# Performance work log

Measured on AMD Instinct MI355X. Metric: run time of the kernel, lower is better.

Reference implementation:

```python
import jax, jax.numpy as jnp
import numpy as np

HEAD_SIZE = 64
N_EMBD = 1024
B, T = 8, 2048

def setup_inputs() -> dict:
    key = jax.random.key(0)
    kx, kq, kk, kv = jax.random.split(key, 4)
    x = jax.random.normal(kx, (B, T, N_EMBD), dtype=jnp.float32)
    s = 1.0 / np.sqrt(N_EMBD)
    Wq = jax.random.normal(kq, (N_EMBD, HEAD_SIZE), dtype=jnp.float32) * s
    Wk = jax.random.normal(kk, (N_EMBD, HEAD_SIZE), dtype=jnp.float32) * s
    Wv = jax.random.normal(kv, (N_EMBD, HEAD_SIZE), dtype=jnp.float32) * s
    return {"x": x, "Wq": Wq, "Wk": Wk, "Wv": Wv}

def reference(x, Wq, Wk, Wv):
    # x: [B,T,C]; project to q,k,v: [B,T,H]
    q = jnp.einsum('btc,ch->bth', x, Wq)
    k = jnp.einsum('btc,ch->bth', x, Wk)
    v = jnp.einsum('btc,ch->bth', x, Wv)
    scale = 1.0 / jnp.sqrt(jnp.asarray(HEAD_SIZE, dtype=x.dtype))
    wei = jnp.einsum('bth,bsh->bts', q, k) * scale  # [B,T,T]
    Tlen = x.shape[1]
    causal = jnp.tril(jnp.ones((Tlen, Tlen), dtype=bool))
    wei = jnp.where(causal[None, :, :], wei, jnp.asarray(-jnp.inf, dtype=wei.dtype))
    wei = jax.nn.softmax(wei, axis=-1)
    # dropout p=0.0 (eval) -> identity
    out = jnp.einsum('bts,bsh->bth', wei, v)  # [B,T,H]
    return out
```

## Files before the change

kernel.cpp:

```cpp
#include <hip/hip_runtime.h>
#include <math.h>

static constexpr int BN = 8;
static constexpr int TS = 2048;
static constexpr int CE = 1024;
static constexpr int HD = 64;

typedef __attribute__((ext_vector_type(8))) short bf16x8;
typedef __attribute__((ext_vector_type(4))) float f32x4;

typedef __attribute__((address_space(3))) void lds_void;
typedef __attribute__((address_space(1))) void glb_void;

__device__ __forceinline__ unsigned short f2bf(float f) {
    union { float f; unsigned u; } v; v.f = f;
    unsigned r = v.u + 0x7FFF + ((v.u >> 16) & 1);
    return (unsigned short)(r >> 16);
}

__device__ __forceinline__ bf16x8 pack8(const float4& a, const float4& b) {
    union { unsigned u[4]; bf16x8 v; } r;
    asm("v_cvt_pk_bf16_f32 %0, %1, %2" : "=v"(r.u[0]) : "v"(a.x), "v"(a.y));
    asm("v_cvt_pk_bf16_f32 %0, %1, %2" : "=v"(r.u[1]) : "v"(a.z), "v"(a.w));
    asm("v_cvt_pk_bf16_f32 %0, %1, %2" : "=v"(r.u[2]) : "v"(b.x), "v"(b.y));
    asm("v_cvt_pk_bf16_f32 %0, %1, %2" : "=v"(r.u[3]) : "v"(b.z), "v"(b.w));
    return r.v;
}

__global__ __launch_bounds__(256) void wt_kernel(
    const float* __restrict__ Wq, const float* __restrict__ Wk,
    const float* __restrict__ Wv, unsigned short* __restrict__ Wt)
{
    __shared__ float T[64 * 69];
    const int tid = threadIdx.x;
    const int m  = blockIdx.x >> 4;
    const int kt = blockIdx.x & 15;
    const float* W = (m == 0) ? Wq : (m == 1) ? Wk : Wv;
    const int k0 = kt * 64;

    #pragma unroll
    for (int it = 0; it < 4; ++it) {
        int idx = tid + it * 256;
        int r = idx >> 4, nq = idx & 15;
        float4 v = *(const float4*)(W + (long)(k0 + r) * HD + nq * 4);
        T[r * 69 + nq * 4 + 0] = v.x;
        T[r * 69 + nq * 4 + 1] = v.y;
        T[r * 69 + nq * 4 + 2] = v.z;
        T[r * 69 + nq * 4 + 3] = v.w;
    }
    __syncthreads();
    #pragma unroll
    for (int it = 0; it < 2; ++it) {
        int idx = tid + it * 256;
        int n = idx >> 3, kq = idx & 7;
        unsigned short h[8];
        #pragma unroll
        for (int s = 0; s < 8; ++s)
            h[s] = f2bf(T[(kq * 8 + s) * 69 + n]);
        *(uint4*)(Wt + (long)(m * 64 + n) * CE + k0 + kq * 8) = *(uint4*)h;
    }
}

static constexpr int NTI = CE / 64;

__global__ __launch_bounds__(512, 1) void qkv_mfma_kernel(
    const float* __restrict__ x, const unsigned short* __restrict__ Wt,
    unsigned short* __restrict__ qo, unsigned short* __restrict__ ko,
    unsigned short* __restrict__ vo)
{
    __shared__ __align__(16) float          xR[4][32 * 64];
    __shared__ __align__(16) unsigned short wR[4][192 * 64];

    const int tid = threadIdx.x;
    const int l  = tid & 63;
    const int v  = tid >> 6;
    const int lr = l & 15, h = l >> 4;
    const int wr = v >> 2;
    const int wc = v & 3;
    const long row0 = (long)blockIdx.x * 32;

    const int sr = tid >> 4;
    const int gd = tid & 15;
    const float* xsrc = x + (row0 + sr) * CE + (gd ^ (2 * (sr & 7))) * 4;
    const int xdst = v << 8;

    const unsigned short* wsrc0; const unsigned short* wsrc1;
    const unsigned short* wsrc2;
    int wdst0, wdst1, wdst2;
    {
        int G, rw, g8;
        G = tid;        rw = G >> 3; g8 = G & 7;
        wsrc0 = Wt + (long)rw * CE + (g8 ^ (rw & 7)) * 8;
        wdst0 = (0 * 512 + v * 64) * 8;
        G = 512 + tid;  rw = G >> 3; g8 = G & 7;
        wsrc1 = Wt + (long)rw * CE + (g8 ^ (rw & 7)) * 8;
        wdst1 = (1 * 512 + v * 64) * 8;
        G = 1024 + tid; rw = G >> 3; g8 = G & 7;
        wsrc2 = Wt + (long)rw * CE + (g8 ^ (rw & 7)) * 8;
        wdst2 = (2 * 512 + v * 64) * 8;
    }

    f32x4 acc[3];
    #pragma unroll
    for (int j = 0; j < 3; ++j) acc[j] = (f32x4){0.f, 0.f, 0.f, 0.f};

    #define STAGE(nb, t) do {                                                 \
        __builtin_amdgcn_global_load_lds((const glb_void*)(xsrc + (t) * 64),  \
            (lds_void*)(&xR[nb][xdst]), 16, 0, 0);                            \
        __builtin_amdgcn_global_load_lds((const glb_void*)(wsrc0 + (t) * 64), \
            (lds_void*)(&wR[nb][wdst0]), 16, 0, 0);                           \
        __builtin_amdgcn_global_load_lds((const glb_void*)(wsrc1 + (t) * 64), \
            (lds_void*)(&wR[nb][wdst1]), 16, 0, 0);                           \
        __builtin_amdgcn_global_load_lds((const glb_void*)(wsrc2 + (t) * 64), \
            (lds_void*)(&wR[nb][wdst2]), 16, 0, 0);                           \
        __builtin_amdgcn_sched_barrier(0); } while (0)

    #define COMPUTE(cb) do {                                                  \
        _Pragma("unroll")                                                     \
        for (int kk = 0; kk < 2; ++kk) {                                      \
            const int xg = (kk * 8 + 2 * h) ^ (2 * (lr & 7));                 \
            const float* ap = &xR[cb][(16 * wr + lr) * 64 + xg * 4];          \
            float4 a0 = *(const float4*)ap;                                   \
            float4 a1 = *(const float4*)(ap + 4);                             \
            bf16x8 af = pack8(a0, a1);                                        \
            _Pragma("unroll")                                                 \
            for (int j = 0; j < 3; ++j) {                                     \
                const int rwj = 48 * wc + 16 * j + lr;                        \
                const int wg  = (kk * 4 + h) ^ (lr & 7);                      \
                bf16x8 bf = *(const bf16x8*)(&wR[cb][rwj * 64 + wg * 8]);     \
                acc[j] = __builtin_amdgcn_mfma_f32_16x16x32_bf16(             \
                    af, bf, acc[j], 0, 0, 0);                                 \
            }                                                                 \
        } } while (0)

    STAGE(0, 0);
    STAGE(1, 1);
    STAGE(2, 2);

    #pragma unroll
    for (int t = 0; t < NTI; ++t) {
        const int cb = t & 3;
        if (t + 3 < NTI) STAGE((t + 3) & 3, t + 3);
        if      (t <  NTI - 3) asm volatile("s_waitcnt vmcnt(12)" ::: "memory");
        else if (t == NTI - 3) asm volatile("s_waitcnt vmcnt(8)"  ::: "memory");
        else if (t == NTI - 2) asm volatile("s_waitcnt vmcnt(4)"  ::: "memory");
        else                   asm volatile("s_waitcnt vmcnt(0)"  ::: "memory");
        __builtin_amdgcn_s_barrier();
        asm volatile("" ::: "memory");
        COMPUTE(cb);
        __builtin_amdgcn_s_barrier();
    }
    #undef STAGE
    #undef COMPUTE

    #pragma unroll
    for (int j = 0; j < 3; ++j) {
        const int n0 = 48 * wc + 16 * j;
        if (n0 < 128) {
            unsigned short* outp = (n0 < 64) ? qo : ko;
            const int h0 = (n0 & 63) + lr;
            #pragma unroll
            for (int r = 0; r < 4; ++r) {
                long rowg = row0 + 16 * wr + h * 4 + r;
                outp[rowg * HD + h0] = f2bf(acc[j][r]);
            }
        } else {
            const int d  = (n0 - 128) + lr;
            const int bb = (int)(row0 >> 11);
            const int t0 = (int)(row0 & 2047) + 16 * wr + h * 4;
            unsigned short h4[4];
            #pragma unroll
            for (int r = 0; r < 4; ++r) h4[r] = f2bf(acc[j][r]);
            *(uint2*)(vo + (((long)(bb * 64 + d)) << 11) + t0) = *(uint2*)h4;
        }
    }
}

__global__ __launch_bounds__(256) void attn_mfma_kernel(
    const unsigned short* __restrict__ qg,
    const unsigned short* __restrict__ kg,
    const unsigned short* __restrict__ vtg,
    float* __restrict__ out)
{
    __shared__ unsigned short Pl[4][32 * 72];
    __shared__ float Ow[4][32 * 64];
    __shared__ float Ml[4][32], Ll[4][32];

    const int tid = threadIdx.x;
    const int w  = tid >> 6;
    const int l  = tid & 63;
    const int lr = l & 15, h = l >> 4;
    const int b  = blockIdx.x >> 5;
    const int pr = blockIdx.x & 31;

    const unsigned short* qB = qg  + (long)b * TS * HD;
    const unsigned short* kB = kg  + (long)b * TS * HD;
    const unsigned short* vT = vtg + (long)b * HD * TS;
    float* outB = out + (long)b * TS * HD;

    unsigned short* Pw = &Pl[w][0];

    for (int half = 0; half < 2; ++half) {
        const int qt = half ? (63 - pr) : pr;
        const int q0 = qt * 32;
        const int NT = (qt + 2) >> 1;

        bf16x8 Qf[2][2];
        #pragma unroll
        for (int qf = 0; qf < 2; ++qf)
            #pragma unroll
            for (int ks = 0; ks < 2; ++ks)
                Qf[qf][ks] = *(const bf16x8*)(qB + (q0 + 16 * qf + lr) * HD + 32 * ks + 8 * h);

        f32x4 O[2][4];
        #pragma unroll
        for (int rf = 0; rf < 2; ++rf)
            #pragma unroll
            for (int cf = 0; cf < 4; ++cf)
                O[rf][cf] = (f32x4){0.f, 0.f, 0.f, 0.f};
        float mrow[2] = {-1e30f, -1e30f};
        float lrow[2] = {0.f, 0.f};

        for (int kt = w; kt < NT; kt += 4) {
            const int key0 = kt * 64;
            bf16x8 Kf[4][2], Vf[4][2];
            #pragma unroll
            for (int kf = 0; kf < 4; ++kf)
                #pragma unroll
                for (int ks = 0; ks < 2; ++ks)
                    Kf[kf][ks] = *(const bf16x8*)(kB + (key0 + 16 * kf + lr) * HD + 32 * ks + 8 * h);
            #pragma unroll
            for (int cf = 0; cf < 4; ++cf)
                #pragma unroll
                for (int ks = 0; ks < 2; ++ks)
                    Vf[cf][ks] = *(const bf16x8*)(vT + (16 * cf + lr) * TS + key0 + 32 * ks + 8 * h);

            f32x4 st[4][2];
            #pragma unroll
            for (int kf = 0; kf < 4; ++kf)
                #pragma unroll
                for (int qf = 0; qf < 2; ++qf)
                    st[kf][qf] = (f32x4){0.f, 0.f, 0.f, 0.f};
            #pragma unroll
            for (int ks = 0; ks < 2; ++ks)
                #pragma unroll
                for (int kf = 0; kf < 4; ++kf)
                    #pragma unroll
                    for (int qf = 0; qf < 2; ++qf)
                        st[kf][qf] = __builtin_amdgcn_mfma_f32_16x16x32_bf16(
                            Kf[kf][ks], Qf[qf][ks], st[kf][qf], 0, 0, 0);

            const bool lastt = (kt == NT - 1);
            float alpha[2];
            #pragma unroll
            for (int qf = 0; qf < 2; ++qf) {
                const int qrow = q0 + 16 * qf + lr;
                float tm = -1e30f;
                #pragma unroll
                for (int kf = 0; kf < 4; ++kf)
                    #pragma unroll
                    for (int r = 0; r < 4; ++r) {
                        float sv = st[kf][qf][r] * 0.125f;
                        if (lastt && (key0 + 16 * kf + 4 * h + r) > qrow) sv = -1e30f;
                        st[kf][qf][r] = sv;
                        tm = fmaxf(tm, sv);
                    }
                tm = fmaxf(tm, __shfl_xor(tm, 16));
                tm = fmaxf(tm, __shfl_xor(tm, 32));
                const float mn = fmaxf(mrow[qf], tm);
                alpha[qf] = __expf(mrow[qf] - mn);
                mrow[qf] = mn;
                float rs = 0.f;
                #pragma unroll
                for (int kf = 0; kf < 4; ++kf)
                    #pragma unroll
                    for (int r = 0; r < 4; ++r) {
                        float p = __expf(st[kf][qf][r] - mn);
                        st[kf][qf][r] = p;
                        rs += p;
                    }
                rs += __shfl_xor(rs, 16);
                rs += __shfl_xor(rs, 32);
                lrow[qf] = lrow[qf] * alpha[qf] + rs;
                #pragma unroll
                for (int kf = 0; kf < 4; ++kf) {
                    unsigned a01 = (unsigned)f2bf(st[kf][qf][0]) |
                                   ((unsigned)f2bf(st[kf][qf][1]) << 16);
                    unsigned a23 = (unsigned)f2bf(st[kf][qf][2]) |
                                   ((unsigned)f2bf(st[kf][qf][3]) << 16);
                    unsigned short* pp = Pw + (16 * qf + lr) * 72 + 16 * kf + 4 * h;
                    *(unsigned*)(pp)     = a01;
                    *(unsigned*)(pp + 2) = a23;
                }
            }

            #pragma unroll
            for (int rf = 0; rf < 2; ++rf)
                #pragma unroll
                for (int r = 0; r < 4; ++r) {
                    float aO = __shfl(alpha[rf], 4 * h + r);
                    #pragma unroll
                    for (int cf = 0; cf < 4; ++cf)
                        O[rf][cf][r] *= aO;
                }

            bf16x8 pa[2][2];
            #pragma unroll
            for (int rf = 0; rf < 2; ++rf)
                #pragma unroll
                for (int ks = 0; ks < 2; ++ks)
                    pa[rf][ks] = *(const bf16x8*)(Pw + (16 * rf + lr) * 72 + 32 * ks + 8 * h);
            #pragma unroll
            for (int ks = 0; ks < 2; ++ks)
                #pragma unroll
                for (int rf = 0; rf < 2; ++rf)
                    #pragma unroll
                    for (int cf = 0; cf < 4; ++cf)
                        O[rf][cf] = __builtin_amdgcn_mfma_f32_16x16x32_bf16(
                            pa[rf][ks], Vf[cf][ks], O[rf][cf], 0, 0, 0);
        }

        #pragma unroll
        for (int rf = 0; rf < 2; ++rf)
            #pragma unroll
            for (int cf = 0; cf < 4; ++cf)
                #pragma unroll
                for (int r = 0; r < 4; ++r)
                    Ow[w][(16 * rf + 4 * h + r) * 64 + 16 * cf + lr] = O[rf][cf][r];
        if (h == 0) {
            #pragma unroll
            for (int qf = 0; qf < 2; ++qf) {
                Ml[w][16 * qf + lr] = mrow[qf];
                Ll[w][16 * qf + lr] = lrow[qf];
            }
        }
        __syncthreads();

        {
            const int q  = tid >> 3;
            const int d0 = (tid & 7) * 8;
            float mM = -1e30f;
            #pragma unroll
            for (int w2 = 0; w2 < 4; ++w2) mM = fmaxf(mM, Ml[w2][q]);
            float lS = 0.f;
            float a8[8] = {0.f,0.f,0.f,0.f,0.f,0.f,0.f,0.f};
            #pragma unroll
            for (int w2 = 0; w2 < 4; ++w2) {
                float sc = __expf(Ml[w2][q] - mM);
                lS += Ll[w2][q] * sc;
                #pragma unroll
                for (int e = 0; e < 8; ++e)
                    a8[e] += sc * Ow[w2][q * 64 + d0 + e];
            }
            const float inv = 1.f / lS;
            float4 o1 = {a8[0]*inv, a8[1]*inv, a8[2]*inv, a8[3]*inv};
            float4 o2 = {a8[4]*inv, a8[5]*inv, a8[6]*inv, a8[7]*inv};
            *(float4*)(outB + (long)(q0 + q) * HD + d0)     = o1;
            *(float4*)(outB + (long)(q0 + q) * HD + d0 + 4) = o2;
        }
        __syncthreads();
    }
}

extern "C" void kernel_launch(void* const* d_in, const int* in_sizes, int n_in,
                              void* d_out, int out_size, void* d_ws, size_t ws_size,
                              hipStream_t stream) {
    const float* x  = (const float*)d_in[0];
    const float* Wq = (const float*)d_in[1];
    const float* Wk = (const float*)d_in[2];
    const float* Wv = (const float*)d_in[3];
    float* out = (float*)d_out;

    const size_t nqkv = (size_t)BN * TS * HD;
    unsigned short* qb = (unsigned short*)d_ws;
    unsigned short* kb = qb + nqkv;
    unsigned short* vt = kb + nqkv;

    unsigned short* Wt = (unsigned short*)d_out;

    wt_kernel<<<48, 256, 0, stream>>>(Wq, Wk, Wv, Wt);
    qkv_mfma_kernel<<<(BN * TS) / 32, 512, 0, stream>>>(x, Wt, qb, kb, vt);
    attn_mfma_kernel<<<BN * 32, 256, 0, stream>>>(qb, kb, vt, out);
}
```

Before: 61.01 us.

## Double QKV projection row tile to 64 and switch to triple-buffered LDS pipeline

The QKV projection kernel now handles 64 rows of x per block instead of 32, so each wave computes two 16-row MFMA tiles that share every loaded weight fragment. This halves how often the bf16 weight tile is re-fetched from global memory and halves the block count to 256. The LDS ring drops from 4 to 3 buffers, the x swizzle changes, and the next stage is issued after the second barrier instead of before compute. In exchange there are fewer blocks to spread across CUs and a shorter prefetch lead.

```diff
diff --git a/kernel.cpp b/kernel.cpp
--- a/kernel.cpp
+++ b/kernel.cpp
@@ -68,8 +68,8 @@
     unsigned short* __restrict__ qo, unsigned short* __restrict__ ko,
     unsigned short* __restrict__ vo)
 {
-    __shared__ __align__(16) float          xR[4][32 * 64];
-    __shared__ __align__(16) unsigned short wR[4][192 * 64];
+    __shared__ __align__(16) float          xR[3][64 * 64];
+    __shared__ __align__(16) unsigned short wR[3][192 * 64];
 
     const int tid = threadIdx.x;
     const int l  = tid & 63;
@@ -77,59 +77,75 @@
     const int lr = l & 15, h = l >> 4;
     const int wr = v >> 2;
     const int wc = v & 3;
-    const long row0 = (long)blockIdx.x * 32;
-
-    const int sr = tid >> 4;
-    const int gd = tid & 15;
-    const float* xsrc = x + (row0 + sr) * CE + (gd ^ (2 * (sr & 7))) * 4;
-    const int xdst = v << 8;
+    const long row0 = (long)blockIdx.x * 64;
+
+    const float* xsrc0; const float* xsrc1;
+    {
+        int G, r_, gd;
+        G = tid;        r_ = G >> 4; gd = G & 15;
+        xsrc0 = x + (row0 + r_) * CE + (gd ^ (r_ & 15)) * 4;
+        G = 512 + tid;  r_ = G >> 4; gd = G & 15;
+        xsrc1 = x + (row0 + r_) * CE + (gd ^ (r_ & 15)) * 4;
+    }
+    const int xd0 = 256 * v;
+    const int xd1 = 2048 + 256 * v;
 
     const unsigned short* wsrc0; const unsigned short* wsrc1;
     const unsigned short* wsrc2;
-    int wdst0, wdst1, wdst2;
     {
         int G, rw, g8;
-        G = tid;        rw = G >> 3; g8 = G & 7;
+        G = tid;         rw = G >> 3; g8 = G & 7;
         wsrc0 = Wt + (long)rw * CE + (g8 ^ (rw & 7)) * 8;
-        wdst0 = (0 * 512 + v * 64) * 8;
-        G = 512 + tid;  rw = G >> 3; g8 = G & 7;
+        G = 512 + tid;   rw = G >> 3; g8 = G & 7;
         wsrc1 = Wt + (long)rw * CE + (g8 ^ (rw & 7)) * 8;
-        wdst1 = (1 * 512 + v * 64) * 8;
-        G = 1024 + tid; rw = G >> 3; g8 = G & 7;
+        G = 1024 + tid;  rw = G >> 3; g8 = G & 7;
         wsrc2 = Wt + (long)rw * CE + (g8 ^ (rw & 7)) * 8;
-        wdst2 = (2 * 512 + v * 64) * 8;
-    }
-
-    f32x4 acc[3];
+    }
+    const int wd0 = 512 * v;
+    const int wd1 = 4096 + 512 * v;
+    const int wd2 = 8192 + 512 * v;
+
+    f32x4 acc[2][3];
     #pragma unroll
-    for (int j = 0; j < 3; ++j) acc[j] = (f32x4){0.f, 0.f, 0.f, 0.f};
+    for (int i = 0; i < 2; ++i)
+        #pragma unroll
+        for (int j = 0; j < 3; ++j)
+            acc[i][j] = (f32x4){0.f, 0.f, 0.f, 0.f};
 
     #define STAGE(nb, t) do {                                                 \
-        __builtin_amdgcn_global_load_lds((const glb_void*)(xsrc + (t) * 64),  \
-            (lds_void*)(&xR[nb][xdst]), 16, 0, 0);                            \
+        __builtin_amdgcn_global_load_lds((const glb_void*)(xsrc0 + (t) * 64), \
+            (lds_void*)(&xR[nb][xd0]), 16, 0, 0);                             \
+        __builtin_amdgcn_global_load_lds((const glb_void*)(xsrc1 + (t) * 64), \
+            (lds_void*)(&xR[nb][xd1]), 16, 0, 0);                             \
         __builtin_amdgcn_global_load_lds((const glb_void*)(wsrc0 + (t) * 64), \
-            (lds_void*)(&wR[nb][wdst0]), 16, 0, 0);                           \
+            (lds_void*)(&wR[nb][wd0]), 16, 0, 0);                             \
         __builtin_amdgcn_global_load_lds((const glb_void*)(wsrc1 + (t) * 64), \
-            (lds_void*)(&wR[nb][wdst1]), 16, 0, 0);                           \
+            (lds_void*)(&wR[nb][wd1]), 16, 0, 0);                             \
         __builtin_amdgcn_global_load_lds((const glb_void*)(wsrc2 + (t) * 64), \
-            (lds_void*)(&wR[nb][wdst2]), 16, 0, 0);                           \
+            (lds_void*)(&wR[nb][wd2]), 16, 0, 0);                             \
         __builtin_amdgcn_sched_barrier(0); } while (0)
 
     #define COMPUTE(cb) do {                                                  \
         _Pragma("unroll")                                                     \
         for (int kk = 0; kk < 2; ++kk) {                                      \
-            const int xg = (kk * 8 + 2 * h) ^ (2 * (lr & 7));                 \
-            const float* ap = &xR[cb][(16 * wr + lr) * 64 + xg * 4];          \
-            float4 a0 = *(const float4*)ap;                                   \
-            float4 a1 = *(const float4*)(ap + 4);                             \
-            bf16x8 af = pack8(a0, a1);                                        \
+            const int g0 = kk * 8 + 2 * h;                                    \
+            bf16x8 af[2];                                                     \
+            _Pragma("unroll")                                                 \
+            for (int i = 0; i < 2; ++i) {                                     \
+                const int rowi = 32 * wr + 16 * i + lr;                       \
+                float4 a0 = *(const float4*)(&xR[cb][rowi * 64 + ((g0    ) ^ lr) * 4]); \
+                float4 a1 = *(const float4*)(&xR[cb][rowi * 64 + ((g0 + 1) ^ lr) * 4]); \
+                af[i] = pack8(a0, a1);                                        \
+            }                                                                 \
             _Pragma("unroll")                                                 \
             for (int j = 0; j < 3; ++j) {                                     \
-                const int rwj = 48 * wc + 16 * j + lr;                        \
-                const int wg  = (kk * 4 + h) ^ (lr & 7);                      \
-                bf16x8 bf = *(const bf16x8*)(&wR[cb][rwj * 64 + wg * 8]);     \
-                acc[j] = __builtin_amdgcn_mfma_f32_16x16x32_bf16(             \
-                    af, bf, acc[j], 0, 0, 0);                                 \
+                const int roww = 48 * wc + 16 * j + lr;                       \
+                const int gw = (kk * 4 + h) ^ (lr & 7);                       \
+                bf16x8 bf = *(const bf16x8*)(&wR[cb][roww * 64 + gw * 8]);    \
+                _Pragma("unroll")                                             \
+                for (int i = 0; i < 2; ++i)                                   \
+                    acc[i][j] = __builtin_amdgcn_mfma_f32_16x16x32_bf16(      \
+                        af[i], bf, acc[i][j], 0, 0, 0);                       \
             }                                                                 \
         } } while (0)
 
@@ -139,16 +155,15 @@
 
     #pragma unroll
     for (int t = 0; t < NTI; ++t) {
-        const int cb = t & 3;
-        if (t + 3 < NTI) STAGE((t + 3) & 3, t + 3);
-        if      (t <  NTI - 3) asm volatile("s_waitcnt vmcnt(12)" ::: "memory");
-        else if (t == NTI - 3) asm volatile("s_waitcnt vmcnt(8)"  ::: "memory");
-        else if (t == NTI - 2) asm volatile("s_waitcnt vmcnt(4)"  ::: "memory");
+        const int cb = t % 3;
+        if      (t <= NTI - 3) asm volatile("s_waitcnt vmcnt(10)" ::: "memory");
+        else if (t == NTI - 2) asm volatile("s_waitcnt vmcnt(5)"  ::: "memory");
         else                   asm volatile("s_waitcnt vmcnt(0)"  ::: "memory");
         __builtin_amdgcn_s_barrier();
         asm volatile("" ::: "memory");
         COMPUTE(cb);
         __builtin_amdgcn_s_barrier();
+        if (t + 3 < NTI) STAGE(cb, t + 3);
     }
     #undef STAGE
     #undef COMPUTE
@@ -160,18 +175,23 @@
             unsigned short* outp = (n0 < 64) ? qo : ko;
             const int h0 = (n0 & 63) + lr;
             #pragma unroll
-            for (int r = 0; r < 4; ++r) {
-                long rowg = row0 + 16 * wr + h * 4 + r;
-                outp[rowg * HD + h0] = f2bf(acc[j][r]);
-            }
+            for (int i = 0; i < 2; ++i)
+                #pragma unroll
+                for (int r = 0; r < 4; ++r) {
+                    long rowg = row0 + 32 * wr + 16 * i + h * 4 + r;
+                    outp[rowg * HD + h0] = f2bf(acc[i][j][r]);
+                }
         } else {
             const int d  = (n0 - 128) + lr;
             const int bb = (int)(row0 >> 11);
-            const int t0 = (int)(row0 & 2047) + 16 * wr + h * 4;
-            unsigned short h4[4];
-            #pragma unroll
-            for (int r = 0; r < 4; ++r) h4[r] = f2bf(acc[j][r]);
-            *(uint2*)(vo + (((long)(bb * 64 + d)) << 11) + t0) = *(uint2*)h4;
+            #pragma unroll
+            for (int i = 0; i < 2; ++i) {
+                const int t0 = (int)(row0 & 2047) + 32 * wr + 16 * i + h * 4;
+                unsigned short h4[4];
+                #pragma unroll
+                for (int r = 0; r < 4; ++r) h4[r] = f2bf(acc[i][j][r]);
+                *(uint2*)(vo + (((long)(bb * 64 + d)) << 11) + t0) = *(uint2*)h4;
+            }
         }
     }
 }
@@ -379,6 +399,6 @@
     unsigned short* Wt = (unsigned short*)d_out;
 
     wt_kernel<<<48, 256, 0, stream>>>(Wq, Wk, Wv, Wt);
-    qkv_mfma_kernel<<<(BN * TS) / 32, 512, 0, stream>>>(x, Wt, qb, kb, vt);
+    qkv_mfma_kernel<<<(BN * TS) / 64, 512, 0, stream>>>(x, Wt, qb, kb, vt);
     attn_mfma_kernel<<<BN * 32, 256, 0, stream>>>(qb, kb, vt, out);
 }
```

Result: faster. 51.13 us (-16.2%).
